# Kernel tuning notes

Hardware: AMD Instinct MI355X
Metric: run time of the kernel (lower is better)

## Reference

```python
import jax, jax.numpy as jnp
import numpy as np

N_NODES = 100000
N_EDGES = 1600000
N_GRAPHS = 64
F_IN = 128
F_HID = 128
F_OUT = 2


def setup_inputs() -> dict:
    key = jax.random.key(0)
    ks = jax.random.split(key, 14)
    p = lambda k, sh: (jax.random.normal(k, sh, jnp.float32) * 0.05)
    return {
        "x": jax.random.normal(ks[0], (N_NODES, F_IN), jnp.float32),
        "edge_index": jax.random.randint(ks[1], (2, N_EDGES), 0, N_NODES),
        "batch": jnp.sort(jax.random.randint(ks[2], (N_NODES,), 0, N_GRAPHS)),
        "W1": p(ks[3], (F_IN, F_HID)),  "b1": jnp.zeros((F_HID,), jnp.float32),
        "W2": p(ks[4], (F_HID, F_HID)), "b2": jnp.zeros((F_HID,), jnp.float32),
        "W3": p(ks[5], (F_HID, F_HID)), "b3": jnp.zeros((F_HID,), jnp.float32),
        "Wp1": p(ks[6], (F_HID, F_HID)), "bp1": jnp.zeros((F_HID,), jnp.float32),
        "Wp2": p(ks[7], (F_HID, F_OUT)), "bp2": jnp.zeros((F_OUT,), jnp.float32),
    }


def reference(x, edge_index, batch, W1, b1, W2, b2, W3, b3, Wp1, bp1, Wp2, bp2):
    n = x.shape[0]
    # GCNConv: add self-loops, symmetric normalization deg^-1/2 A_hat deg^-1/2
    loops = jnp.arange(n)
    src = jnp.concatenate([edge_index[0], loops])
    dst = jnp.concatenate([edge_index[1], loops])
    deg = jax.ops.segment_sum(jnp.ones(src.shape, x.dtype), dst, num_segments=n)
    dinv = jax.lax.rsqrt(deg)  # deg >= 1 due to self-loops
    norm = dinv[src] * dinv[dst]  # [E+N]

    def gcn_conv(h, W, b):
        hl = h @ W                          # [N, F']
        msg = hl[src] * norm[:, None]       # gather + scale, [E+N, F']
        return jax.ops.segment_sum(msg, dst, num_segments=n) + b

    h = x
    for W, b in ((W1, b1), (W2, b2), (W3, b3)):
        h = jax.nn.relu(gcn_conv(h, W, b))  # dropout is identity in eval mode

    pooled = jax.ops.segment_max(h, batch, num_segments=N_GRAPHS)  # [G, F_HID]
    logits = (pooled @ Wp1 + bp1) @ Wp2 + bp2                      # [G, F_OUT]
    return jax.nn.log_softmax(logits, axis=1)
```

## Files before the change

### kernel.cpp

```cpp
#include <hip/hip_runtime.h>

#define F 128
#define PSH 13
#define NP 13
#define DPW 10

typedef __attribute__((ext_vector_type(8))) short bf16x8;
typedef __attribute__((ext_vector_type(4))) float f32x4;
typedef __attribute__((ext_vector_type(2))) float vf2;

#if defined(__has_builtin)
#if __has_builtin(__builtin_amdgcn_cvt_pk_f32_fp8) && __has_builtin(__builtin_amdgcn_cvt_pk_fp8_f32)
#define HW_FP8 1
#endif
#endif


__device__ __forceinline__ unsigned short f32_to_bf16_rne(float x) {
    unsigned u = __float_as_uint(x);
    unsigned r = (u + 0x7fffu + ((u >> 16) & 1u)) >> 16;
    return (unsigned short)r;
}

__device__ __forceinline__ float bfhi(unsigned v) { return __uint_as_float(v & 0xffff0000u); }
__device__ __forceinline__ float bflo(unsigned v) { return __uint_as_float(v << 16); }


__device__ __forceinline__ unsigned char f32_to_fp8(float x) {
#ifdef HW_FP8
    int p = __builtin_amdgcn_cvt_pk_fp8_f32(x, x, 0, false);
    return (unsigned char)(p & 0xFF);
#else
    float ax = fminf(fabsf(x), 448.0f);
    unsigned s = (__float_as_uint(x) >> 31) << 7;
    if (ax < 0.0009765625f) return (unsigned char)s;
    int e;
    float mant = frexpf(ax, &e);
    int E = e - 1;
    unsigned bits;
    if (E < -6) {
        bits = (unsigned)rintf(ax * 512.0f);
    } else {
        unsigned m = (unsigned)rintf((2.0f * mant - 1.0f) * 8.0f);
        unsigned ee = (unsigned)(E + 7);
        if (m == 8) { m = 0; ee += 1; }
        if (ee >= 15 && (ee > 15 || m >= 7)) { ee = 15; m = 6; }
        bits = (ee << 3) | m;
    }
    return (unsigned char)(s | bits);
#endif
}

__device__ __forceinline__ float2 fp8x2_to_f32(unsigned short v) {
#ifdef HW_FP8
    vf2 r = __builtin_amdgcn_cvt_pk_f32_fp8((int)(unsigned)v, false);
    return make_float2(r[0], r[1]);
#else
    float2 o;
    #pragma unroll
    for (int i = 0; i < 2; i++) {
        unsigned b = (v >> (8 * i)) & 0xFF;
        unsigned s = b >> 7, e = (b >> 3) & 15, m = b & 7;
        float fn = __uint_as_float((s << 31) | ((e + 120) << 23) | (m << 20));
        float fd = (s ? -1.0f : 1.0f) * (float)m * 0.001953125f;
        float val = e ? fn : fd;
        if (i == 0) o.x = val; else o.y = val;
    }
    return o;
#endif
}


__global__ __launch_bounds__(256) void cvtx_kernel(const float4* __restrict__ x4,
                                                   ushort4* __restrict__ xb4, long n4) {
    long stride = (long)gridDim.x * 256;
    for (long i = blockIdx.x * 256 + threadIdx.x; i < n4; i += stride) {
        float4 v = x4[i];
        ushort4 o;
        o.x = f32_to_bf16_rne(v.x);
        o.y = f32_to_bf16_rne(v.y);
        o.z = f32_to_bf16_rne(v.z);
        o.w = f32_to_bf16_rne(v.w);
        xb4[i] = o;
    }
}

__global__ __launch_bounds__(128) void cvtw_kernel(const float* __restrict__ W,
                                                   unsigned short* __restrict__ Wt) {
    int c = blockIdx.x, k = threadIdx.x;
    Wt[c * F + k] = f32_to_bf16_rne(W[k * F + c]);
}


__global__ __launch_bounds__(256) void gemm_mfma(const unsigned short* __restrict__ hb,
                                                 const unsigned short* __restrict__ Wt,
                                                 unsigned char* __restrict__ outb8, int n) {
    __shared__ unsigned char smb[4][16][F];
    const int tid = threadIdx.x;
    const int w = tid >> 6, lane = tid & 63;
    const int r = lane & 15, kg = lane >> 4;
    const long base = (long)blockIdx.x * 64 + w * 16;

    int arow = (int)(base + r);
    if (arow >= n) arow = n - 1;
    const bf16x8* __restrict__ arowp = (const bf16x8*)(hb + (size_t)arow * F);

    f32x4 acc[8] = {};
    #pragma unroll
    for (int c = 0; c < 4; c++) {
        bf16x8 a = arowp[c * 4 + kg];
        #pragma unroll
        for (int t = 0; t < 8; t++) {
            bf16x8 b = *(const bf16x8*)(Wt + (size_t)(t * 16 + r) * F + c * 32 + kg * 8);
            acc[t] = __builtin_amdgcn_mfma_f32_16x16x32_bf16(a, b, acc[t], 0, 0, 0);
        }
    }

    #pragma unroll
    for (int t = 0; t < 8; t++)
        #pragma unroll
        for (int j = 0; j < 4; j++)
            smb[w][kg * 4 + j][t * 16 + r] = f32_to_fp8(acc[t][j]);
    #pragma unroll
    for (int it = 0; it < 4; it++) {
        int row = it * 4 + kg;
        long grow = base + row;
        if (grow < n) {
            uint2 v = *(uint2*)&smb[w][row][r * 8];
            *(uint2*)(outb8 + (size_t)grow * F + r * 8) = v;
        }
    }
}


__global__ __launch_bounds__(256) void count16_kernel(const int* __restrict__ src,
                                                      const int* __restrict__ dst,
                                                      int* __restrict__ cnt,
                                                      int* __restrict__ cntd, int e) {
    int i = blockIdx.x * 256 + threadIdx.x;
    if (i >= e) return;
    int s = src[i], d = dst[i];
    unsigned p = (unsigned)s >> PSH;
    atomicAdd(&cnt[(size_t)((unsigned)d / DPW) * NP + p], 1);
    atomicAdd(&cntd[d], 1);
}

__global__ __launch_bounds__(256) void dinv_kernel(const int* __restrict__ cnt,
                                                   float* __restrict__ dinv, int n) {
    int i = blockIdx.x * 256 + threadIdx.x;
    if (i < n) dinv[i] = rsqrtf((float)(cnt[i] + 1));
}

__global__ __launch_bounds__(256) void scanA_kernel(const int* __restrict__ cnt,
                                                    int* __restrict__ bsum, int M) {
    __shared__ int sm[256];
    int t = threadIdx.x;
    int i = blockIdx.x * 256 + t;
    int v = (i < M) ? cnt[i] : 0;
    sm[t] = v;
    __syncthreads();
    for (int d = 128; d > 0; d >>= 1) {
        if (t < d) sm[t] += sm[t + d];
        __syncthreads();
    }
    if (t == 0) bsum[blockIdx.x] = sm[0];
}

__global__ __launch_bounds__(1024) void scanB_kernel(const int* __restrict__ bsum,
                                                     int* __restrict__ bpre,
                                                     int* __restrict__ offs, int nb, int M) {
    __shared__ int sm[1024];
    int t = threadIdx.x;
    int chunk = (nb + 1023) >> 10;
    int b = t * chunk;
    int e = b + chunk; if (e > nb) e = nb;
    int s = 0;
    for (int i = b; i < e; i++) s += bsum[i];
    sm[t] = s;
    __syncthreads();
    for (int d = 1; d < 1024; d <<= 1) {
        int v = 0;
        if (t >= d) v = sm[t - d];
        __syncthreads();
        if (t >= d) sm[t] += v;
        __syncthreads();
    }
    int run = (t == 0) ? 0 : sm[t - 1];
    for (int i = b; i < e; i++) { bpre[i] = run; run += bsum[i]; }
    if (t == 1023) offs[M] = sm[1023];
}

__global__ __launch_bounds__(256) void scanC_kernel(const int* __restrict__ cnt,
                                                    const int* __restrict__ bpre,
                                                    int* __restrict__ offs, int M) {
    __shared__ int sm[256];
    int t = threadIdx.x;
    int i = blockIdx.x * 256 + t;
    int v = (i < M) ? cnt[i] : 0;
    sm[t] = v;
    __syncthreads();
    for (int d = 1; d < 256; d <<= 1) {
        int u = 0;
        if (t >= d) u = sm[t - d];
        __syncthreads();
        if (t >= d) sm[t] += u;
        __syncthreads();
    }
    if (i < M) offs[i] = bpre[blockIdx.x] + sm[t] - v;
}

__global__ __launch_bounds__(256) void fill16_kernel(const int* __restrict__ src,
                                                     const int* __restrict__ dst,
                                                     const int* __restrict__ offs,
                                                     int* __restrict__ cur,
                                                     const float* __restrict__ dinv,
                                                     int2* __restrict__ csr, int e) {
    int i = blockIdx.x * 256 + threadIdx.x;
    if (i >= e) return;
    int s = src[i], d = dst[i];
    unsigned p = (unsigned)s >> PSH;
    unsigned wq = (unsigned)d / DPW;
    unsigned dm = (unsigned)d - wq * DPW;
    size_t bin = (size_t)wq * NP + p;
    int pos = offs[bin] + atomicAdd(&cur[bin], 1);
    csr[pos] = make_int2(s | (dm << 20), __float_as_int(dinv[s] * dinv[d]));
}


#define RMW(fk, nk, dk)                                              \
    {                                                                \
        float2 t = acc2[wbase + (dk)][lane];                         \
        t.x += fk.x * (nk);                                          \
        t.y += fk.y * (nk);                                          \
        acc2[wbase + (dk)][lane] = t;                                \
    }

template <int POOL>
__global__ __launch_bounds__(512) void aggL_kernel(const unsigned short* __restrict__ hl8,
                                                   const int* __restrict__ offs,
                                                   const int2* __restrict__ csr,
                                                   const float* __restrict__ dinv,
                                                   const float* __restrict__ bias,
                                                   void* __restrict__ outp,
                                                   const int* __restrict__ batch,
                                                   int n, int nwq) {
    __shared__ float2 acc2[8 * DPW][64];
    const int lane = threadIdx.x & 63;
    const int w = __builtin_amdgcn_readfirstlane(threadIdx.x >> 6);
    const int wq = blockIdx.x * 8 + w;
    const int wbase = w * DPW;
    const float2 bv = ((const float2*)bias)[lane];
    if (wq >= nwq) return;

    #pragma unroll
    for (int dl = 0; dl < DPW; dl++)
        acc2[wbase + dl][lane] = make_float2(0.0f, 0.0f);

    const int e0 = offs[wq * NP];
    const int e1 = offs[wq * NP + NP];
    int e = e0;
    int nb = (e1 - e0) >> 3;

    int2 c0, c1, c2, c3, c4, c5, c6, c7;
    if (nb > 0) {
        c0 = csr[e + 0]; c1 = csr[e + 1]; c2 = csr[e + 2]; c3 = csr[e + 3];
        c4 = csr[e + 4]; c5 = csr[e + 5]; c6 = csr[e + 6]; c7 = csr[e + 7];
    }
    for (int b = 0; b < nb; b++) {
        unsigned short r0 = hl8[((size_t)(c0.x & 0xFFFFF) << 6) + lane];
        unsigned short r1 = hl8[((size_t)(c1.x & 0xFFFFF) << 6) + lane];
        unsigned short r2 = hl8[((size_t)(c2.x & 0xFFFFF) << 6) + lane];
        unsigned short r3 = hl8[((size_t)(c3.x & 0xFFFFF) << 6) + lane];
        unsigned short r4 = hl8[((size_t)(c4.x & 0xFFFFF) << 6) + lane];
        unsigned short r5 = hl8[((size_t)(c5.x & 0xFFFFF) << 6) + lane];
        unsigned short r6 = hl8[((size_t)(c6.x & 0xFFFFF) << 6) + lane];
        unsigned short r7 = hl8[((size_t)(c7.x & 0xFFFFF) << 6) + lane];
        float n0 = __int_as_float(c0.y), n1 = __int_as_float(c1.y);
        float n2 = __int_as_float(c2.y), n3 = __int_as_float(c3.y);
        float n4 = __int_as_float(c4.y), n5 = __int_as_float(c5.y);
        float n6 = __int_as_float(c6.y), n7 = __int_as_float(c7.y);
        int d0 = (unsigned)c0.x >> 20, d1 = (unsigned)c1.x >> 20;
        int d2 = (unsigned)c2.x >> 20, d3 = (unsigned)c3.x >> 20;
        int d4 = (unsigned)c4.x >> 20, d5 = (unsigned)c5.x >> 20;
        int d6 = (unsigned)c6.x >> 20, d7 = (unsigned)c7.x >> 20;
        e += 8;
        if (b + 1 < nb) {
            c0 = csr[e + 0]; c1 = csr[e + 1]; c2 = csr[e + 2]; c3 = csr[e + 3];
            c4 = csr[e + 4]; c5 = csr[e + 5]; c6 = csr[e + 6]; c7 = csr[e + 7];
        }
        float2 f0 = fp8x2_to_f32(r0), f1 = fp8x2_to_f32(r1);
        float2 f2 = fp8x2_to_f32(r2), f3 = fp8x2_to_f32(r3);
        float2 f4 = fp8x2_to_f32(r4), f5 = fp8x2_to_f32(r5);
        float2 f6 = fp8x2_to_f32(r6), f7 = fp8x2_to_f32(r7);
        RMW(f0, n0, d0); RMW(f1, n1, d1); RMW(f2, n2, d2); RMW(f3, n3, d3);
        RMW(f4, n4, d4); RMW(f5, n5, d5); RMW(f6, n6, d6); RMW(f7, n7, d7);
    }
    for (; e < e1; e++) {
        int2 c = csr[e];
        float2 f = fp8x2_to_f32(hl8[((size_t)(c.x & 0xFFFFF) << 6) + lane]);
        float nf = __int_as_float(c.y);
        int dl = (unsigned)c.x >> 20;
        RMW(f, nf, dl);
    }

    #pragma unroll
    for (int dl = 0; dl < DPW; dl++) {
        int d = wq * DPW + dl;
        if (d < n) {
            float2 t = acc2[wbase + dl][lane];
            float di = dinv[d];
            float sw = di * di;
            float2 sv = fp8x2_to_f32(hl8[((size_t)d << 6) + lane]);
            float rx = fmaxf(t.x + sv.x * sw + bv.x, 0.0f);
            float ry = fmaxf(t.y + sv.y * sw + bv.y, 0.0f);
            if (POOL) {
                int g = batch[d];
                float* out = (float*)outp;
                atomicMax((int*)&out[(size_t)g * F + 2 * lane + 0], __float_as_int(rx));
                atomicMax((int*)&out[(size_t)g * F + 2 * lane + 1], __float_as_int(ry));
            } else {
                unsigned lo = (unsigned)f32_to_bf16_rne(rx);
                unsigned hi = (unsigned)f32_to_bf16_rne(ry);
                ((unsigned*)outp)[((size_t)d << 6) + lane] = lo | (hi << 16);
            }
        }
    }
}


__global__ __launch_bounds__(128) void mlp_kernel(const float* __restrict__ pooled,
                                                  const float* __restrict__ Wp1,
                                                  const float* __restrict__ bp1,
                                                  const float* __restrict__ Wp2,
                                                  const float* __restrict__ bp2,
                                                  float* __restrict__ out) {
    __shared__ float pl[F];
    __shared__ float s0[2], s1[2];
    int g = blockIdx.x, t = threadIdx.x;
    pl[t] = pooled[(size_t)g * F + t];
    __syncthreads();
    float a = bp1[t];
    #pragma unroll 8
    for (int k = 0; k < F; k++) a += pl[k] * Wp1[k * F + t];
    float p0 = a * Wp2[t * 2 + 0];
    float p1 = a * Wp2[t * 2 + 1];
    #pragma unroll
    for (int d = 32; d > 0; d >>= 1) {
        p0 += __shfl_down(p0, d, 64);
        p1 += __shfl_down(p1, d, 64);
    }
    if ((t & 63) == 0) { s0[t >> 6] = p0; s1[t >> 6] = p1; }
    __syncthreads();
    if (t == 0) {
        float l0 = s0[0] + s0[1] + bp2[0];
        float l1 = s1[0] + s1[1] + bp2[1];
        float m = fmaxf(l0, l1);
        float lse = m + logf(expf(l0 - m) + expf(l1 - m));
        out[g * 2 + 0] = l0 - lse;
        out[g * 2 + 1] = l1 - lse;
    }
}


extern "C" void kernel_launch(void* const* d_in, const int* in_sizes, int n_in,
                              void* d_out, int out_size, void* d_ws, size_t ws_size,
                              hipStream_t stream) {
    const float* x    = (const float*)d_in[0];
    const int*   ei   = (const int*)d_in[1];
    const int*   batch= (const int*)d_in[2];
    const float* W1 = (const float*)d_in[3];  const float* b1 = (const float*)d_in[4];
    const float* W2 = (const float*)d_in[5];  const float* b2 = (const float*)d_in[6];
    const float* W3 = (const float*)d_in[7];  const float* b3 = (const float*)d_in[8];
    const float* Wp1= (const float*)d_in[9];  const float* bp1= (const float*)d_in[10];
    const float* Wp2= (const float*)d_in[11]; const float* bp2= (const float*)d_in[12];

    const int N = in_sizes[0] / F;
    const int E = in_sizes[1] / 2;
    const int G = out_size / 2;
    const int* srcp = ei;
    const int* dstp = ei + E;
    const int eb = (E + 255) / 256;
    const int nb = (N + 255) / 256;

    const int nwq = (N + DPW - 1) / DPW;
    const int nblocks = (nwq + 7) / 8;
    const size_t M = (size_t)nwq * NP;
    const int nblkM = (int)((M + 255) / 256);

    char* w = (char*)d_ws;
    size_t off = 0;
    auto alloc = [&](size_t bytes) -> void* {
        void* p = w + off;
        off = (off + bytes + 255) & ~(size_t)255;
        return p;
    };
    unsigned short* xb   = (unsigned short*)alloc((size_t)N * F * 2);
    unsigned char*  hl8  = (unsigned char*)alloc((size_t)N * F);
    unsigned short* hab  = (unsigned short*)alloc((size_t)N * F * 2);
    unsigned short* Wt1  = (unsigned short*)alloc((size_t)F * F * 2);
    unsigned short* Wt2  = (unsigned short*)alloc((size_t)F * F * 2);
    unsigned short* Wt3  = (unsigned short*)alloc((size_t)F * F * 2);
    int*   cnt16  = (int*)alloc(M * 4);
    int*   cur16  = (int*)alloc(M * 4);
    int*   offs16 = (int*)alloc((M + 1) * 4);
    int*   bsum   = (int*)alloc((size_t)nblkM * 4);
    int*   bpre   = (int*)alloc((size_t)nblkM * 4);
    int*   cntd   = (int*)alloc((size_t)N * 4);
    float* dinv   = (float*)alloc((size_t)N * 4);
    int2*  csr16  = (int2*)alloc((size_t)E * 8);
    float* pooled = (float*)alloc((size_t)G * F * 4);

    hipMemsetAsync(cnt16, 0, M * 4, stream);
    hipMemsetAsync(cur16, 0, M * 4, stream);
    hipMemsetAsync(cntd,  0, (size_t)N * 4, stream);
    hipMemsetAsync(pooled, 0, (size_t)G * F * 4, stream);

    cvtx_kernel<<<2048, 256, 0, stream>>>((const float4*)x, (ushort4*)xb, (long)N * F / 4);
    cvtw_kernel<<<F, F, 0, stream>>>(W1, Wt1);
    cvtw_kernel<<<F, F, 0, stream>>>(W2, Wt2);
    cvtw_kernel<<<F, F, 0, stream>>>(W3, Wt3);

    count16_kernel<<<eb, 256, 0, stream>>>(srcp, dstp, cnt16, cntd, E);
    dinv_kernel<<<nb, 256, 0, stream>>>(cntd, dinv, N);
    scanA_kernel<<<nblkM, 256, 0, stream>>>(cnt16, bsum, (int)M);
    scanB_kernel<<<1, 1024, 0, stream>>>(bsum, bpre, offs16, nblkM, (int)M);
    scanC_kernel<<<nblkM, 256, 0, stream>>>(cnt16, bpre, offs16, (int)M);
    fill16_kernel<<<eb, 256, 0, stream>>>(srcp, dstp, offs16, cur16, dinv, csr16, E);

    const int gb = (N + 63) / 64;

    gemm_mfma<<<gb, 256, 0, stream>>>(xb, Wt1, hl8, N);
    aggL_kernel<0><<<nblocks, 512, 0, stream>>>((const unsigned short*)hl8, offs16, csr16, dinv, b1, hab, nullptr, N, nwq);
    gemm_mfma<<<gb, 256, 0, stream>>>(hab, Wt2, hl8, N);
    aggL_kernel<0><<<nblocks, 512, 0, stream>>>((const unsigned short*)hl8, offs16, csr16, dinv, b2, hab, nullptr, N, nwq);
    gemm_mfma<<<gb, 256, 0, stream>>>(hab, Wt3, hl8, N);
    aggL_kernel<1><<<nblocks, 512, 0, stream>>>((const unsigned short*)hl8, offs16, csr16, dinv, b3, pooled, batch, N, nwq);

    mlp_kernel<<<G, 128, 0, stream>>>(pooled, Wp1, bp1, Wp2, bp2, (float*)d_out);
}
```

Before: 622.0 us.

## Fuse input bf16 conversion into first GEMM and make aggregation grid-stride

The standalone fp32-to-bf16 conversion pass over x is removed. The first MFMA GEMM now reads fp32 rows directly and converts them to bf16 in registers through a template flag, which drops a full write and re-read of a bf16 copy of x and one kernel launch. The aggregation kernel also becomes a persistent grid-stride loop with a fixed grid of 1024 blocks instead of one block per 8 wave-work-items. With 1024 blocks some waves process two work items, so the tail may be less balanced than before.

```diff
diff --git a/kernel.cpp b/kernel.cpp
--- a/kernel.cpp
+++ b/kernel.cpp
@@ -4,6 +4,7 @@
 #define PSH 13
 #define NP 13
 #define DPW 10
+#define AGRID 1024
 
 typedef __attribute__((ext_vector_type(8))) short bf16x8;
 typedef __attribute__((ext_vector_type(4))) float f32x4;
@@ -71,20 +72,6 @@
 }
 
 
-__global__ __launch_bounds__(256) void cvtx_kernel(const float4* __restrict__ x4,
-                                                   ushort4* __restrict__ xb4, long n4) {
-    long stride = (long)gridDim.x * 256;
-    for (long i = blockIdx.x * 256 + threadIdx.x; i < n4; i += stride) {
-        float4 v = x4[i];
-        ushort4 o;
-        o.x = f32_to_bf16_rne(v.x);
-        o.y = f32_to_bf16_rne(v.y);
-        o.z = f32_to_bf16_rne(v.z);
-        o.w = f32_to_bf16_rne(v.w);
-        xb4[i] = o;
-    }
-}
-
 __global__ __launch_bounds__(128) void cvtw_kernel(const float* __restrict__ W,
                                                    unsigned short* __restrict__ Wt) {
     int c = blockIdx.x, k = threadIdx.x;
@@ -92,7 +79,8 @@
 }
 
 
-__global__ __launch_bounds__(256) void gemm_mfma(const unsigned short* __restrict__ hb,
+template <int F32IN>
+__global__ __launch_bounds__(256) void gemm_mfma(const void* __restrict__ hin,
                                                  const unsigned short* __restrict__ Wt,
                                                  unsigned char* __restrict__ outb8, int n) {
     __shared__ unsigned char smb[4][16][F];
@@ -103,12 +91,26 @@
 
     int arow = (int)(base + r);
     if (arow >= n) arow = n - 1;
-    const bf16x8* __restrict__ arowp = (const bf16x8*)(hb + (size_t)arow * F);
 
     f32x4 acc[8] = {};
     #pragma unroll
     for (int c = 0; c < 4; c++) {
-        bf16x8 a = arowp[c * 4 + kg];
+        bf16x8 a;
+        if (F32IN) {
+            const float* ap = (const float*)hin + (size_t)arow * F + c * 32 + kg * 8;
+            float4 v0 = *(const float4*)ap;
+            float4 v1 = *(const float4*)(ap + 4);
+            a[0] = (short)f32_to_bf16_rne(v0.x);
+            a[1] = (short)f32_to_bf16_rne(v0.y);
+            a[2] = (short)f32_to_bf16_rne(v0.z);
+            a[3] = (short)f32_to_bf16_rne(v0.w);
+            a[4] = (short)f32_to_bf16_rne(v1.x);
+            a[5] = (short)f32_to_bf16_rne(v1.y);
+            a[6] = (short)f32_to_bf16_rne(v1.z);
+            a[7] = (short)f32_to_bf16_rne(v1.w);
+        } else {
+            a = ((const bf16x8*)((const unsigned short*)hin + (size_t)arow * F))[c * 4 + kg];
+        }
         #pragma unroll
         for (int t = 0; t < 8; t++) {
             bf16x8 b = *(const bf16x8*)(Wt + (size_t)(t * 16 + r) * F + c * 32 + kg * 8);
@@ -247,81 +249,81 @@
     __shared__ float2 acc2[8 * DPW][64];
     const int lane = threadIdx.x & 63;
     const int w = __builtin_amdgcn_readfirstlane(threadIdx.x >> 6);
-    const int wq = blockIdx.x * 8 + w;
     const int wbase = w * DPW;
     const float2 bv = ((const float2*)bias)[lane];
-    if (wq >= nwq) return;
-
-    #pragma unroll
-    for (int dl = 0; dl < DPW; dl++)
-        acc2[wbase + dl][lane] = make_float2(0.0f, 0.0f);
-
-    const int e0 = offs[wq * NP];
-    const int e1 = offs[wq * NP + NP];
-    int e = e0;
-    int nb = (e1 - e0) >> 3;
-
-    int2 c0, c1, c2, c3, c4, c5, c6, c7;
-    if (nb > 0) {
-        c0 = csr[e + 0]; c1 = csr[e + 1]; c2 = csr[e + 2]; c3 = csr[e + 3];
-        c4 = csr[e + 4]; c5 = csr[e + 5]; c6 = csr[e + 6]; c7 = csr[e + 7];
-    }
-    for (int b = 0; b < nb; b++) {
-        unsigned short r0 = hl8[((size_t)(c0.x & 0xFFFFF) << 6) + lane];
-        unsigned short r1 = hl8[((size_t)(c1.x & 0xFFFFF) << 6) + lane];
-        unsigned short r2 = hl8[((size_t)(c2.x & 0xFFFFF) << 6) + lane];
-        unsigned short r3 = hl8[((size_t)(c3.x & 0xFFFFF) << 6) + lane];
-        unsigned short r4 = hl8[((size_t)(c4.x & 0xFFFFF) << 6) + lane];
-        unsigned short r5 = hl8[((size_t)(c5.x & 0xFFFFF) << 6) + lane];
-        unsigned short r6 = hl8[((size_t)(c6.x & 0xFFFFF) << 6) + lane];
-        unsigned short r7 = hl8[((size_t)(c7.x & 0xFFFFF) << 6) + lane];
-        float n0 = __int_as_float(c0.y), n1 = __int_as_float(c1.y);
-        float n2 = __int_as_float(c2.y), n3 = __int_as_float(c3.y);
-        float n4 = __int_as_float(c4.y), n5 = __int_as_float(c5.y);
-        float n6 = __int_as_float(c6.y), n7 = __int_as_float(c7.y);
-        int d0 = (unsigned)c0.x >> 20, d1 = (unsigned)c1.x >> 20;
-        int d2 = (unsigned)c2.x >> 20, d3 = (unsigned)c3.x >> 20;
-        int d4 = (unsigned)c4.x >> 20, d5 = (unsigned)c5.x >> 20;
-        int d6 = (unsigned)c6.x >> 20, d7 = (unsigned)c7.x >> 20;
-        e += 8;
-        if (b + 1 < nb) {
+
+    for (int wq = blockIdx.x * 8 + w; wq < nwq; wq += AGRID * 8) {
+        #pragma unroll
+        for (int dl = 0; dl < DPW; dl++)
+            acc2[wbase + dl][lane] = make_float2(0.0f, 0.0f);
+
+        const int e0 = offs[wq * NP];
+        const int e1 = offs[wq * NP + NP];
+        int e = e0;
+        int nb = (e1 - e0) >> 3;
+
+        int2 c0, c1, c2, c3, c4, c5, c6, c7;
+        if (nb > 0) {
             c0 = csr[e + 0]; c1 = csr[e + 1]; c2 = csr[e + 2]; c3 = csr[e + 3];
             c4 = csr[e + 4]; c5 = csr[e + 5]; c6 = csr[e + 6]; c7 = csr[e + 7];
         }
-        float2 f0 = fp8x2_to_f32(r0), f1 = fp8x2_to_f32(r1);
-        float2 f2 = fp8x2_to_f32(r2), f3 = fp8x2_to_f32(r3);
-        float2 f4 = fp8x2_to_f32(r4), f5 = fp8x2_to_f32(r5);
-        float2 f6 = fp8x2_to_f32(r6), f7 = fp8x2_to_f32(r7);
-        RMW(f0, n0, d0); RMW(f1, n1, d1); RMW(f2, n2, d2); RMW(f3, n3, d3);
-        RMW(f4, n4, d4); RMW(f5, n5, d5); RMW(f6, n6, d6); RMW(f7, n7, d7);
-    }
-    for (; e < e1; e++) {
-        int2 c = csr[e];
-        float2 f = fp8x2_to_f32(hl8[((size_t)(c.x & 0xFFFFF) << 6) + lane]);
-        float nf = __int_as_float(c.y);
-        int dl = (unsigned)c.x >> 20;
-        RMW(f, nf, dl);
-    }
-
-    #pragma unroll
-    for (int dl = 0; dl < DPW; dl++) {
-        int d = wq * DPW + dl;
-        if (d < n) {
-            float2 t = acc2[wbase + dl][lane];
-            float di = dinv[d];
-            float sw = di * di;
-            float2 sv = fp8x2_to_f32(hl8[((size_t)d << 6) + lane]);
-            float rx = fmaxf(t.x + sv.x * sw + bv.x, 0.0f);
-            float ry = fmaxf(t.y + sv.y * sw + bv.y, 0.0f);
-            if (POOL) {
-                int g = batch[d];
-                float* out = (float*)outp;
-                atomicMax((int*)&out[(size_t)g * F + 2 * lane + 0], __float_as_int(rx));
-                atomicMax((int*)&out[(size_t)g * F + 2 * lane + 1], __float_as_int(ry));
-            } else {
-                unsigned lo = (unsigned)f32_to_bf16_rne(rx);
-                unsigned hi = (unsigned)f32_to_bf16_rne(ry);
-                ((unsigned*)outp)[((size_t)d << 6) + lane] = lo | (hi << 16);
+        for (int b = 0; b < nb; b++) {
+            unsigned short r0 = hl8[((size_t)(c0.x & 0xFFFFF) << 6) + lane];
+            unsigned short r1 = hl8[((size_t)(c1.x & 0xFFFFF) << 6) + lane];
+            unsigned short r2 = hl8[((size_t)(c2.x & 0xFFFFF) << 6) + lane];
+            unsigned short r3 = hl8[((size_t)(c3.x & 0xFFFFF) << 6) + lane];
+            unsigned short r4 = hl8[((size_t)(c4.x & 0xFFFFF) << 6) + lane];
+            unsigned short r5 = hl8[((size_t)(c5.x & 0xFFFFF) << 6) + lane];
+            unsigned short r6 = hl8[((size_t)(c6.x & 0xFFFFF) << 6) + lane];
+            unsigned short r7 = hl8[((size_t)(c7.x & 0xFFFFF) << 6) + lane];
+            float n0 = __int_as_float(c0.y), n1 = __int_as_float(c1.y);
+            float n2 = __int_as_float(c2.y), n3 = __int_as_float(c3.y);
+            float n4 = __int_as_float(c4.y), n5 = __int_as_float(c5.y);
+            float n6 = __int_as_float(c6.y), n7 = __int_as_float(c7.y);
+            int d0 = (unsigned)c0.x >> 20, d1 = (unsigned)c1.x >> 20;
+            int d2 = (unsigned)c2.x >> 20, d3 = (unsigned)c3.x >> 20;
+            int d4 = (unsigned)c4.x >> 20, d5 = (unsigned)c5.x >> 20;
+            int d6 = (unsigned)c6.x >> 20, d7 = (unsigned)c7.x >> 20;
+            e += 8;
+            if (b + 1 < nb) {
+                c0 = csr[e + 0]; c1 = csr[e + 1]; c2 = csr[e + 2]; c3 = csr[e + 3];
+                c4 = csr[e + 4]; c5 = csr[e + 5]; c6 = csr[e + 6]; c7 = csr[e + 7];
+            }
+            float2 f0 = fp8x2_to_f32(r0), f1 = fp8x2_to_f32(r1);
+            float2 f2 = fp8x2_to_f32(r2), f3 = fp8x2_to_f32(r3);
+            float2 f4 = fp8x2_to_f32(r4), f5 = fp8x2_to_f32(r5);
+            float2 f6 = fp8x2_to_f32(r6), f7 = fp8x2_to_f32(r7);
+            RMW(f0, n0, d0); RMW(f1, n1, d1); RMW(f2, n2, d2); RMW(f3, n3, d3);
+            RMW(f4, n4, d4); RMW(f5, n5, d5); RMW(f6, n6, d6); RMW(f7, n7, d7);
+        }
+        for (; e < e1; e++) {
+            int2 c = csr[e];
+            float2 f = fp8x2_to_f32(hl8[((size_t)(c.x & 0xFFFFF) << 6) + lane]);
+            float nf = __int_as_float(c.y);
+            int dl = (unsigned)c.x >> 20;
+            RMW(f, nf, dl);
+        }
+
+        #pragma unroll
+        for (int dl = 0; dl < DPW; dl++) {
+            int d = wq * DPW + dl;
+            if (d < n) {
+                float2 t = acc2[wbase + dl][lane];
+                float di = dinv[d];
+                float sw = di * di;
+                float2 sv = fp8x2_to_f32(hl8[((size_t)d << 6) + lane]);
+                float rx = fmaxf(t.x + sv.x * sw + bv.x, 0.0f);
+                float ry = fmaxf(t.y + sv.y * sw + bv.y, 0.0f);
+                if (POOL) {
+                    int g = batch[d];
+                    float* out = (float*)outp;
+                    atomicMax((int*)&out[(size_t)g * F + 2 * lane + 0], __float_as_int(rx));
+                    atomicMax((int*)&out[(size_t)g * F + 2 * lane + 1], __float_as_int(ry));
+                } else {
+                    unsigned lo = (unsigned)f32_to_bf16_rne(rx);
+                    unsigned hi = (unsigned)f32_to_bf16_rne(ry);
+                    ((unsigned*)outp)[((size_t)d << 6) + lane] = lo | (hi << 16);
+                }
             }
         }
     }
@@ -383,7 +385,6 @@
     const int nb = (N + 255) / 256;
 
     const int nwq = (N + DPW - 1) / DPW;
-    const int nblocks = (nwq + 7) / 8;
     const size_t M = (size_t)nwq * NP;
     const int nblkM = (int)((M + 255) / 256);
 
@@ -394,7 +395,6 @@
         off = (off + bytes + 255) & ~(size_t)255;
         return p;
     };
-    unsigned short* xb   = (unsigned short*)alloc((size_t)N * F * 2);
     unsigned char*  hl8  = (unsigned char*)alloc((size_t)N * F);
     unsigned short* hab  = (unsigned short*)alloc((size_t)N * F * 2);
     unsigned short* Wt1  = (unsigned short*)alloc((size_t)F * F * 2);
@@ -415,7 +415,6 @@
     hipMemsetAsync(cntd,  0, (size_t)N * 4, stream);
     hipMemsetAsync(pooled, 0, (size_t)G * F * 4, stream);
 
-    cvtx_kernel<<<2048, 256, 0, stream>>>((const float4*)x, (ushort4*)xb, (long)N * F / 4);
     cvtw_kernel<<<F, F, 0, stream>>>(W1, Wt1);
     cvtw_kernel<<<F, F, 0, stream>>>(W2, Wt2);
     cvtw_kernel<<<F, F, 0, stream>>>(W3, Wt3);
@@ -429,12 +428,12 @@
 
     const int gb = (N + 63) / 64;
 
-    gemm_mfma<<<gb, 256, 0, stream>>>(xb, Wt1, hl8, N);
-    aggL_kernel<0><<<nblocks, 512, 0, stream>>>((const unsigned short*)hl8, offs16, csr16, dinv, b1, hab, nullptr, N, nwq);
-    gemm_mfma<<<gb, 256, 0, stream>>>(hab, Wt2, hl8, N);
-    aggL_kernel<0><<<nblocks, 512, 0, stream>>>((const unsigned short*)hl8, offs16, csr16, dinv, b2, hab, nullptr, N, nwq);
-    gemm_mfma<<<gb, 256, 0, stream>>>(hab, Wt3, hl8, N);
-    aggL_kernel<1><<<nblocks, 512, 0, stream>>>((const unsigned short*)hl8, offs16, csr16, dinv, b3, pooled, batch, N, nwq);
+    gemm_mfma<1><<<gb, 256, 0, stream>>>(x, Wt1, hl8, N);
+    aggL_kernel<0><<<AGRID, 512, 0, stream>>>((const unsigned short*)hl8, offs16, csr16, dinv, b1, hab, nullptr, N, nwq);
+    gemm_mfma<0><<<gb, 256, 0, stream>>>(hab, Wt2, hl8, N);
+    aggL_kernel<0><<<AGRID, 512, 0, stream>>>((const unsigned short*)hl8, offs16, csr16, dinv, b2, hab, nullptr, N, nwq);
+    gemm_mfma<0><<<gb, 256, 0, stream>>>(hab, Wt3, hl8, N);
+    aggL_kernel<1><<<AGRID, 512, 0, stream>>>((const unsigned short*)hl8, offs16, csr16, dinv, b3, pooled, batch, N, nwq);
 
     mlp_kernel<<<G, 128, 0, stream>>>(pooled, Wp1, bp1, Wp2, bp2, (float*)d_out);
 }
```

After: 584.0 us. -6.1%, faster.
